# Kernel tuning notes

Hardware: AMD Instinct MI355X
Metric: run time of the kernel (lower is better)

Reference implementation:

```python
import jax, jax.numpy as jnp
import numpy as np

N = 16384          # number of units
K = 655
BOOST_STRENGTH = 1.0


def setup_inputs() -> dict:
    key = jax.random.key(0)
    k1, k2 = jax.random.split(key)
    x = jax.random.normal(k1, (4096, N), dtype=jnp.float32)
    dutyCycle = jax.random.uniform(k2, (N,), dtype=jnp.float32)
    return {"x": x, "dutyCycle": dutyCycle}


def reference(x, dutyCycle):
    # boost factor per unit: encourages under-used units
    targetDensity = K / x.shape[1]
    boostFactors = jnp.exp((targetDensity - dutyCycle) * BOOST_STRENGTH)  # (N,)
    boosted = x * boostFactors  # (B, N)
    # top-k per row, then scatter a binary mask of winners
    _, idx = jax.lax.top_k(boosted, K)  # (B, K)
    b = jnp.arange(x.shape[0])[:, None]  # (B, 1)
    res = jnp.zeros_like(x).at[b, idx].set(1.0)
    return res
```

## Files before the change

kernel.cpp:

```cpp
#include <hip/hip_runtime.h>
#include <math.h>
#include <stdint.h>


#define N_UNITS 16384
#define K_WIN 655
#define NT 512
#define NPROBE 5
#define CAP 512

typedef float f32x4 __attribute__((ext_vector_type(4)));

__device__ __forceinline__ uint32_t fkey(float f) {
    uint32_t b = __float_as_uint(f);
    uint32_t m = (uint32_t)((int32_t)b >> 31) | 0x80000000u;
    return b ^ m;
}

__global__ void boost_kernel(const float* __restrict__ duty,
                             float* __restrict__ bf, int n) {
    int i = blockIdx.x * blockDim.x + threadIdx.x;
    if (i < n) {
        const float td = 0.03997802734375f;
        float s = td - duty[i];
        bf[i] = (float)exp((double)s);
    }
}

__global__ __launch_bounds__(NT, 8) void kwinners_kernel(
    const float* __restrict__ x, const float* __restrict__ bf,
    float* __restrict__ out) {
    __shared__ __align__(16) uint32_t khiw[N_UNITS / 2];
    __shared__ uint32_t red[(NT / 64) * NPROBE];
    __shared__ int cglob[NPROBE];
    __shared__ uint32_t cand_idx[CAP];
    __shared__ uint32_t cand_key[CAP];
    __shared__ int prb[NPROBE];
    __shared__ int sc[2];

    const int tid = threadIdx.x;
    const int lane = tid & 63;
    const int w = tid >> 6;
    const int row = blockIdx.x;
    const f32x4* xrow = (const f32x4*)(x + (size_t)row * N_UNITS);
    const f32x4* bfv = (const f32x4*)bf;
    float* orow = out + (size_t)row * N_UNITS;

    if (tid == 0) sc[0] = 0;
    __syncthreads();

    int P[NPROBE] = {0xBFC0, 0xBFA6, 0xBF9A, 0xBF8F, 0xBF66};
    int cnt[NPROBE];
#pragma unroll
    for (int p = 0; p < NPROBE; ++p) cnt[p] = 0;

#pragma unroll
    for (int j = 0; j < N_UNITS / (NT * 4); ++j) {
        int i4 = tid + j * NT;
        f32x4 xv = __builtin_nontemporal_load(xrow + i4);
        f32x4 bv = bfv[i4];
        int h0 = (int)(fkey(xv.x * bv.x) >> 16);
        int h1 = (int)(fkey(xv.y * bv.y) >> 16);
        int h2 = (int)(fkey(xv.z * bv.z) >> 16);
        int h3 = (int)(fkey(xv.w * bv.w) >> 16);
        uint2 pk;
        pk.x = (uint32_t)h0 | ((uint32_t)h1 << 16);
        pk.y = (uint32_t)h2 | ((uint32_t)h3 << 16);
        ((uint2*)khiw)[i4] = pk;
#pragma unroll
        for (int p = 0; p < NPROBE; ++p)
            cnt[p] += (h0 > P[p]) + (h1 > P[p]) + (h2 > P[p]) + (h3 > P[p]);
    }

    auto reduce_counts = [&]() {
#pragma unroll
        for (int p = 0; p < NPROBE; ++p) {
            int v = cnt[p];
#pragma unroll
            for (int m = 32; m >= 1; m >>= 1) v += __shfl_xor(v, m, 64);
            if (lane == 0) red[w * NPROBE + p] = (uint32_t)v;
        }
        __syncthreads();
        if (tid < NPROBE) {
            int s = 0;
#pragma unroll
            for (int ww = 0; ww < NT / 64; ++ww) s += (int)red[ww * NPROBE + tid];
            cglob[tid] = s;
        }
        __syncthreads();
    };
    reduce_counts();

    int lo, hi, cab, cgl;
    {
        int j = 0;
        while (j < NPROBE && cglob[j] < K_WIN) ++j;
        if (j == 0) {
            lo = P[0]; cgl = cglob[0]; hi = 65535; cab = 0;
        } else if (j == NPROBE) {
            lo = -1; cgl = N_UNITS; hi = P[NPROBE - 1]; cab = cglob[NPROBE - 1];
        } else {
            lo = P[j]; cgl = cglob[j]; hi = P[j - 1]; cab = cglob[j - 1];
        }
    }
    int m = cgl - cab;

    while (m > CAP && (hi - lo) > 1) {
        __syncthreads();
        if (tid < NPROBE)
            prb[tid] = lo + (int)(((long)(hi - lo) * (NPROBE - tid)) / (NPROBE + 1));
        __syncthreads();
#pragma unroll
        for (int p = 0; p < NPROBE; ++p) P[p] = prb[p];
#pragma unroll
        for (int p = 0; p < NPROBE; ++p) cnt[p] = 0;
        for (int j = 0; j < 4; ++j) {
            uint4 wv = ((const uint4*)khiw)[tid + j * NT];
            int h0 = (int)(wv.x & 0xFFFFu), h1 = (int)(wv.x >> 16);
            int h2 = (int)(wv.y & 0xFFFFu), h3 = (int)(wv.y >> 16);
            int h4 = (int)(wv.z & 0xFFFFu), h5 = (int)(wv.z >> 16);
            int h6 = (int)(wv.w & 0xFFFFu), h7 = (int)(wv.w >> 16);
#pragma unroll
            for (int p = 0; p < NPROBE; ++p)
                cnt[p] += (h0 > P[p]) + (h1 > P[p]) + (h2 > P[p]) + (h3 > P[p]) +
                          (h4 > P[p]) + (h5 > P[p]) + (h6 > P[p]) + (h7 > P[p]);
        }
        reduce_counts();
        int j = 0;
        while (j < NPROBE && cglob[j] < K_WIN) ++j;
        if (j == 0) {
            lo = P[0]; cgl = cglob[0];
        } else if (j == NPROBE) {
            hi = P[NPROBE - 1]; cab = cglob[NPROBE - 1];
        } else {
            lo = P[j]; cgl = cglob[j]; hi = P[j - 1]; cab = cglob[j - 1];
        }
        m = cgl - cab;
    }

    for (int j = 0; j < N_UNITS / (NT * 4); ++j) {
        int q = tid + j * NT;
        uint2 wv = ((const uint2*)khiw)[q];
        int h0 = (int)(wv.x & 0xFFFFu), h1 = (int)(wv.x >> 16);
        int h2 = (int)(wv.y & 0xFFFFu), h3 = (int)(wv.y >> 16);
        f32x4 o;
        o.x = (h0 > hi) ? 1.0f : 0.0f;
        o.y = (h1 > hi) ? 1.0f : 0.0f;
        o.z = (h2 > hi) ? 1.0f : 0.0f;
        o.w = (h3 > hi) ? 1.0f : 0.0f;
        __builtin_nontemporal_store(o, ((f32x4*)orow) + q);
        int base = q * 4;
        if (h0 > lo && h0 <= hi) {
            int p = atomicAdd(&sc[0], 1);
            if (p < CAP) cand_idx[p] = (uint32_t)(base + 0);
        }
        if (h1 > lo && h1 <= hi) {
            int p = atomicAdd(&sc[0], 1);
            if (p < CAP) cand_idx[p] = (uint32_t)(base + 1);
        }
        if (h2 > lo && h2 <= hi) {
            int p = atomicAdd(&sc[0], 1);
            if (p < CAP) cand_idx[p] = (uint32_t)(base + 2);
        }
        if (h3 > lo && h3 <= hi) {
            int p = atomicAdd(&sc[0], 1);
            if (p < CAP) cand_idx[p] = (uint32_t)(base + 3);
        }
    }
    __syncthreads();
    const int mm = sc[0];
    const int need = K_WIN - cab;

    const float* xr = x + (size_t)row * N_UNITS;
    const int mc = (mm <= CAP) ? mm : 0;
    for (int j = tid; j < mc; j += NT) {
        int i = (int)cand_idx[j];
        cand_key[j] = fkey(xr[i] * bf[i]);
    }
    __syncthreads();

    if (mm <= CAP) {
        for (int j = tid; j < mm; j += NT) {
            uint32_t myk = cand_key[j];
            uint32_t myi = cand_idx[j];
            int r = 0;
            for (int l = 0; l < mm; ++l) {
                uint32_t lk = cand_key[l];
                r += (lk > myk) || (lk == myk && cand_idx[l] < myi);
            }
            if (r < need) orow[myi] = 1.0f;
        }
    } else if (tid == 0) {
        uint32_t* h8 = cand_idx;
        for (int b = 0; b < 256; ++b) h8[b] = 0;
        for (int i = 0; i < N_UNITS; ++i) {
            int h = (int)((khiw[i >> 1] >> ((i & 1) * 16)) & 0xFFFFu);
            if (h == hi) h8[(fkey(xr[i] * bf[i]) & 0xFFFFu) >> 8]++;
        }
        int acc = 0, d1 = 0, need2 = 0;
        for (int b = 255; b >= 0; --b) {
            int c = (int)h8[b];
            if (acc + c >= need) { d1 = b; need2 = need - acc; break; }
            acc += c;
        }
        for (int b = 0; b < 256; ++b) h8[b] = 0;
        for (int i = 0; i < N_UNITS; ++i) {
            int h = (int)((khiw[i >> 1] >> ((i & 1) * 16)) & 0xFFFFu);
            if (h == hi) {
                uint32_t kl = fkey(xr[i] * bf[i]) & 0xFFFFu;
                if ((int)(kl >> 8) == d1) h8[kl & 0xFFu]++;
            }
        }
        int acc2 = 0, d2 = 0, need3 = 0;
        for (int b = 255; b >= 0; --b) {
            int c = (int)h8[b];
            if (acc2 + c >= need2) { d2 = b; need3 = need2 - acc2; break; }
            acc2 += c;
        }
        uint32_t Tlo = ((uint32_t)d1 << 8) | (uint32_t)d2;
        int r = 0;
        for (int i = 0; i < N_UNITS; ++i) {
            int h = (int)((khiw[i >> 1] >> ((i & 1) * 16)) & 0xFFFFu);
            if (h == hi) {
                uint32_t kl = fkey(xr[i] * bf[i]) & 0xFFFFu;
                if (kl > Tlo) orow[i] = 1.0f;
                else if (kl == Tlo && r < need3) { orow[i] = 1.0f; ++r; }
            }
        }
    }
}

extern "C" void kernel_launch(void* const* d_in, const int* in_sizes, int n_in,
                              void* d_out, int out_size, void* d_ws,
                              size_t ws_size, hipStream_t stream) {
    const float* x = (const float*)d_in[0];
    const float* duty = (const float*)d_in[1];
    float* out = (float*)d_out;
    float* bf = (float*)d_ws;

    hipLaunchKernelGGL(boost_kernel, dim3(N_UNITS / 256), dim3(256), 0, stream,
                       duty, bf, N_UNITS);
    int rows = out_size / N_UNITS;
    hipLaunchKernelGGL(kwinners_kernel, dim3(rows), dim3(NT), 0, stream, x, bf,
                       out);
}
```

Baseline: 547.3 us.

## Keep 16-bit keys in registers instead of shared memory, drop nontemporal hints

The packed high-16-bit keys (16 values per thread) now live in a per-thread register array instead of a 32 KB shared buffer, so the refinement and output passes read registers. This cuts LDS use from about 36 KB to a few KB per block, which allows more blocks per CU and avoids LDS traffic. The rare fallback path now recomputes keys from global memory. Nontemporal load and store hints are also replaced with plain accesses, which changes cache behavior for the streamed input and output.

```diff
diff --git a/kernel.cpp b/kernel.cpp
--- a/kernel.cpp
+++ b/kernel.cpp
@@ -8,6 +8,7 @@
 #define NT 512
 #define NPROBE 5
 #define CAP 512
+#define ITERS (N_UNITS / (NT * 4))
 
 typedef float f32x4 __attribute__((ext_vector_type(4)));
 
@@ -30,13 +31,12 @@
 __global__ __launch_bounds__(NT, 8) void kwinners_kernel(
     const float* __restrict__ x, const float* __restrict__ bf,
     float* __restrict__ out) {
-    __shared__ __align__(16) uint32_t khiw[N_UNITS / 2];
     __shared__ uint32_t red[(NT / 64) * NPROBE];
     __shared__ int cglob[NPROBE];
+    __shared__ int prb[NPROBE];
     __shared__ uint32_t cand_idx[CAP];
     __shared__ uint32_t cand_key[CAP];
-    __shared__ int prb[NPROBE];
-    __shared__ int sc[2];
+    __shared__ int sc[1];
 
     const int tid = threadIdx.x;
     const int lane = tid & 63;
@@ -53,23 +53,23 @@
     int cnt[NPROBE];
 #pragma unroll
     for (int p = 0; p < NPROBE; ++p) cnt[p] = 0;
-
-#pragma unroll
-    for (int j = 0; j < N_UNITS / (NT * 4); ++j) {
+    uint32_t kh[ITERS * 2];
+
+#pragma unroll
+    for (int j = 0; j < ITERS; ++j) {
         int i4 = tid + j * NT;
-        f32x4 xv = __builtin_nontemporal_load(xrow + i4);
+        f32x4 xv = xrow[i4];
         f32x4 bv = bfv[i4];
-        int h0 = (int)(fkey(xv.x * bv.x) >> 16);
-        int h1 = (int)(fkey(xv.y * bv.y) >> 16);
-        int h2 = (int)(fkey(xv.z * bv.z) >> 16);
-        int h3 = (int)(fkey(xv.w * bv.w) >> 16);
-        uint2 pk;
-        pk.x = (uint32_t)h0 | ((uint32_t)h1 << 16);
-        pk.y = (uint32_t)h2 | ((uint32_t)h3 << 16);
-        ((uint2*)khiw)[i4] = pk;
+        uint32_t h0 = fkey(xv.x * bv.x) >> 16;
+        uint32_t h1 = fkey(xv.y * bv.y) >> 16;
+        uint32_t h2 = fkey(xv.z * bv.z) >> 16;
+        uint32_t h3 = fkey(xv.w * bv.w) >> 16;
+        kh[2 * j] = h0 | (h1 << 16);
+        kh[2 * j + 1] = h2 | (h3 << 16);
 #pragma unroll
         for (int p = 0; p < NPROBE; ++p)
-            cnt[p] += (h0 > P[p]) + (h1 > P[p]) + (h2 > P[p]) + (h3 > P[p]);
+            cnt[p] += ((int)h0 > P[p]) + ((int)h1 > P[p]) + ((int)h2 > P[p]) +
+                      ((int)h3 > P[p]);
     }
 
     auto reduce_counts = [&]() {
@@ -114,16 +114,15 @@
         for (int p = 0; p < NPROBE; ++p) P[p] = prb[p];
 #pragma unroll
         for (int p = 0; p < NPROBE; ++p) cnt[p] = 0;
-        for (int j = 0; j < 4; ++j) {
-            uint4 wv = ((const uint4*)khiw)[tid + j * NT];
-            int h0 = (int)(wv.x & 0xFFFFu), h1 = (int)(wv.x >> 16);
-            int h2 = (int)(wv.y & 0xFFFFu), h3 = (int)(wv.y >> 16);
-            int h4 = (int)(wv.z & 0xFFFFu), h5 = (int)(wv.z >> 16);
-            int h6 = (int)(wv.w & 0xFFFFu), h7 = (int)(wv.w >> 16);
+#pragma unroll
+        for (int j = 0; j < ITERS; ++j) {
+            int h0 = (int)(kh[2 * j] & 0xFFFFu);
+            int h1 = (int)(kh[2 * j] >> 16);
+            int h2 = (int)(kh[2 * j + 1] & 0xFFFFu);
+            int h3 = (int)(kh[2 * j + 1] >> 16);
 #pragma unroll
             for (int p = 0; p < NPROBE; ++p)
-                cnt[p] += (h0 > P[p]) + (h1 > P[p]) + (h2 > P[p]) + (h3 > P[p]) +
-                          (h4 > P[p]) + (h5 > P[p]) + (h6 > P[p]) + (h7 > P[p]);
+                cnt[p] += (h0 > P[p]) + (h1 > P[p]) + (h2 > P[p]) + (h3 > P[p]);
         }
         reduce_counts();
         int j = 0;
@@ -138,18 +137,20 @@
         m = cgl - cab;
     }
 
-    for (int j = 0; j < N_UNITS / (NT * 4); ++j) {
-        int q = tid + j * NT;
-        uint2 wv = ((const uint2*)khiw)[q];
-        int h0 = (int)(wv.x & 0xFFFFu), h1 = (int)(wv.x >> 16);
-        int h2 = (int)(wv.y & 0xFFFFu), h3 = (int)(wv.y >> 16);
+#pragma unroll
+    for (int j = 0; j < ITERS; ++j) {
+        int i4 = tid + j * NT;
+        int h0 = (int)(kh[2 * j] & 0xFFFFu);
+        int h1 = (int)(kh[2 * j] >> 16);
+        int h2 = (int)(kh[2 * j + 1] & 0xFFFFu);
+        int h3 = (int)(kh[2 * j + 1] >> 16);
         f32x4 o;
         o.x = (h0 > hi) ? 1.0f : 0.0f;
         o.y = (h1 > hi) ? 1.0f : 0.0f;
         o.z = (h2 > hi) ? 1.0f : 0.0f;
         o.w = (h3 > hi) ? 1.0f : 0.0f;
-        __builtin_nontemporal_store(o, ((f32x4*)orow) + q);
-        int base = q * 4;
+        ((f32x4*)orow)[i4] = o;
+        int base = i4 * 4;
         if (h0 > lo && h0 <= hi) {
             int p = atomicAdd(&sc[0], 1);
             if (p < CAP) cand_idx[p] = (uint32_t)(base + 0);
@@ -194,8 +195,8 @@
         uint32_t* h8 = cand_idx;
         for (int b = 0; b < 256; ++b) h8[b] = 0;
         for (int i = 0; i < N_UNITS; ++i) {
-            int h = (int)((khiw[i >> 1] >> ((i & 1) * 16)) & 0xFFFFu);
-            if (h == hi) h8[(fkey(xr[i] * bf[i]) & 0xFFFFu) >> 8]++;
+            uint32_t k = fkey(xr[i] * bf[i]);
+            if ((int)(k >> 16) == hi) h8[(k & 0xFFFFu) >> 8]++;
         }
         int acc = 0, d1 = 0, need2 = 0;
         for (int b = 255; b >= 0; --b) {
@@ -205,11 +206,9 @@
         }
         for (int b = 0; b < 256; ++b) h8[b] = 0;
         for (int i = 0; i < N_UNITS; ++i) {
-            int h = (int)((khiw[i >> 1] >> ((i & 1) * 16)) & 0xFFFFu);
-            if (h == hi) {
-                uint32_t kl = fkey(xr[i] * bf[i]) & 0xFFFFu;
-                if ((int)(kl >> 8) == d1) h8[kl & 0xFFu]++;
-            }
+            uint32_t k = fkey(xr[i] * bf[i]);
+            if ((int)(k >> 16) == hi && (int)((k & 0xFFFFu) >> 8) == d1)
+                h8[k & 0xFFu]++;
         }
         int acc2 = 0, d2 = 0, need3 = 0;
         for (int b = 255; b >= 0; --b) {
@@ -220,9 +219,9 @@
         uint32_t Tlo = ((uint32_t)d1 << 8) | (uint32_t)d2;
         int r = 0;
         for (int i = 0; i < N_UNITS; ++i) {
-            int h = (int)((khiw[i >> 1] >> ((i & 1) * 16)) & 0xFFFFu);
-            if (h == hi) {
-                uint32_t kl = fkey(xr[i] * bf[i]) & 0xFFFFu;
+            uint32_t k = fkey(xr[i] * bf[i]);
+            if ((int)(k >> 16) == hi) {
+                uint32_t kl = k & 0xFFFFu;
                 if (kl > Tlo) orow[i] = 1.0f;
                 else if (kl == Tlo && r < need3) { orow[i] = 1.0f; ++r; }
             }
```

New measurement: 499.2 us. 8.8% less time.
